# Kernel tuning notes

Measured on AMD Instinct MI355X. Metric: run time of the kernel, lower is better.

Reference implementation:

```python
import jax, jax.numpy as jnp
import numpy as np

D_MODEL = 1024
NUM_HEADS = 16
HEAD_DIM = D_MODEL // NUM_HEADS
SCALE = HEAD_DIM ** -0.5


def setup_inputs() -> dict:
    key = jax.random.key(0)
    k1, k2, k3 = jax.random.split(key, 3)
    x = jax.random.normal(k1, (4, 2048, D_MODEL), dtype=jnp.float32)
    # torch Linear stores weight [out, in]; we store transposed [in, out] for x @ W
    w_qkv = jax.random.normal(k2, (D_MODEL, 3 * D_MODEL), dtype=jnp.float32) * (D_MODEL ** -0.5)
    w_out = jax.random.normal(k3, (D_MODEL, D_MODEL), dtype=jnp.float32) * (D_MODEL ** -0.5)
    return {"x": x, "w_qkv": w_qkv, "w_out": w_out}


def reference(x, w_qkv, w_out):
    batch, seq_len, _ = x.shape
    qkv = x @ w_qkv  # [B, S, 3*D]
    q, k, v = jnp.split(qkv, 3, axis=-1)

    def to_heads(t):
        return t.reshape(batch, seq_len, NUM_HEADS, HEAD_DIM).transpose(0, 2, 1, 3)  # [B, H, S, Dh]

    q, k, v = to_heads(q), to_heads(k), to_heads(v)
    attn = jnp.einsum('bhqd,bhkd->bhqk', q, k) * SCALE  # [B, H, S, S]
    causal = jnp.tril(jnp.ones((seq_len, seq_len), dtype=bool))
    attn = jnp.where(causal[None, None], attn, -jnp.inf)
    attn = jax.nn.softmax(attn, axis=-1)
    out = jnp.einsum('bhqk,bhkd->bhqd', attn, v)  # [B, H, S, Dh]
    out = out.transpose(0, 2, 1, 3).reshape(batch, seq_len, D_MODEL)
    return out @ w_out
```

## Files before the change

### kernel.cpp

```cpp
#include <hip/hip_runtime.h>
#include <hip/hip_bf16.h>

typedef unsigned short u16;
typedef float f32x4 __attribute__((ext_vector_type(4)));
typedef __bf16 bf16x8 __attribute__((ext_vector_type(8)));
typedef u16 u16x8 __attribute__((ext_vector_type(8)));
typedef u16 u16x4 __attribute__((ext_vector_type(4)));
typedef unsigned u32x2 __attribute__((ext_vector_type(2)));

__device__ __forceinline__ u16 f2bf(float f) {
  unsigned u = __builtin_bit_cast(unsigned, f);
  u = (u + 0x7fffu + ((u >> 16) & 1u)) >> 16;
  return (u16)u;
}

__device__ __forceinline__ unsigned cvtpk(float lo, float hi) {
  unsigned r;
  asm("v_cvt_pk_bf16_f32 %0, %1, %2" : "=v"(r) : "v"(lo), "v"(hi));
  return r;
}

__device__ __forceinline__ float exp2b(float x) {
  return __builtin_amdgcn_exp2f(x);
}

__device__ __forceinline__ void gload16(const void* g, void* l) {
  __builtin_amdgcn_global_load_lds(
      (const __attribute__((address_space(1))) unsigned*)g,
      (__attribute__((address_space(3))) unsigned*)l, 16, 0, 0);
}

__device__ __forceinline__ f32x4 mfma16(bf16x8 a, bf16x8 b, f32x4 c) {
  return __builtin_amdgcn_mfma_f32_16x16x32_bf16(a, b, c, 0, 0, 0);
}

__global__ __launch_bounds__(256) void convx(const float4* __restrict__ x,
                                             u16x8* __restrict__ xb, int n) {
  int i = blockIdx.x * 256 + threadIdx.x;
  if (i >= n) return;
  float4 a = x[2 * i], b = x[2 * i + 1];
  u16x8 o;
  o[0] = f2bf(a.x); o[1] = f2bf(a.y); o[2] = f2bf(a.z); o[3] = f2bf(a.w);
  o[4] = f2bf(b.x); o[5] = f2bf(b.y); o[6] = f2bf(b.z); o[7] = f2bf(b.w);
  xb[i] = o;
}

__global__ __launch_bounds__(256) void transpose_w(const float* __restrict__ w,
                                                   u16* __restrict__ wt,
                                                   int R, int C) {
  __shared__ float tile[32][33];
  int n0 = blockIdx.x * 32, k0 = blockIdx.y * 32;
  int tx = threadIdx.x & 31, ty = threadIdx.x >> 5;
#pragma unroll
  for (int j = 0; j < 32; j += 8)
    tile[ty + j][tx] = w[(size_t)(k0 + ty + j) * C + n0 + tx];
  __syncthreads();
#pragma unroll
  for (int j = 0; j < 32; j += 8)
    wt[(size_t)(n0 + ty + j) * R + k0 + tx] = f2bf(tile[tx][ty + j]);
}

template <int MODE, int BM, int BN, int WGM, int WGN, int WPE>
__global__ __launch_bounds__(512, WPE) void gemm_t(const u16* __restrict__ A,
                                                   const u16* __restrict__ Bt,
                                                   void* __restrict__ Cv,
                                                   int M, int N, int K,
                                                   u16* __restrict__ Qb,
                                                   u16* __restrict__ Kb) {
  constexpr int PWM = BM / WGM, PWN = BN / WGN;
  constexpr int MI = PWM / 16;
  constexpr bool PH2 = (MI >= 4);
  constexpr int MH = PH2 ? MI / 2 : MI;
  static_assert(PWN == 64, "per-wave N must be 64 (NI=4)");
  constexpr int ALD = BM / 128, BLD = BN / 128, LPT = ALD + BLD;
  __shared__ alignas(16) u16 As[3][BM][32];
  __shared__ alignas(16) u16 Bs[3][BN][32];
  const int tix = threadIdx.x;
  const int lane = tix & 63, wid = tix >> 6;
  const int wm = wid / WGN, wn = wid % WGN;
  const int r = lane & 15, g = lane >> 4;
  const int s2 = (r >> 1) & 3;
  const int m0 = blockIdx.y * BM, n0 = blockIdx.x * BN;

  const int srow = tix >> 2;
  const int swc = (tix & 3) ^ ((srow >> 1) & 3);
  const u16* gA[ALD];
  const u16* gB[BLD];
#pragma unroll
  for (int i = 0; i < ALD; ++i)
    gA[i] = A + (size_t)(m0 + i * 128 + srow) * K + swc * 8;
#pragma unroll
  for (int i = 0; i < BLD; ++i)
    gB[i] = Bt + (size_t)(n0 + i * 128 + srow) * K + swc * 8;

  auto SA = [&](int tt, int bb) {
    const int ko = tt * 32;
#pragma unroll
    for (int i = 0; i < ALD; ++i)
      gload16(gA[i] + ko, &As[bb][i * 128 + wid * 16][0]);
  };
  auto SB = [&](int tt, int bb) {
    const int ko = tt * 32;
#pragma unroll
    for (int i = 0; i < BLD; ++i)
      gload16(gB[i] + ko, &Bs[bb][i * 128 + wid * 16][0]);
  };

  f32x4 acc[MI][4] = {};
  const int NT = K >> 5;

  SA(0, 0); SB(0, 0); SA(1, 1); SB(1, 1);

  int bu = 0;
  for (int t = 0; t < NT; ++t) {
    if (t < NT - 1) {
      if constexpr (LPT == 3) asm volatile("s_waitcnt vmcnt(3)" ::: "memory");
      else                    asm volatile("s_waitcnt vmcnt(2)" ::: "memory");
    } else {
      asm volatile("s_waitcnt vmcnt(0)" ::: "memory");
    }
    __builtin_amdgcn_s_barrier();
    __builtin_amdgcn_sched_barrier(0);

    const int bs = (bu >= 1) ? bu - 1 : 2;

    bf16x8 a0[MH], bf[4];
#pragma unroll
    for (int mi = 0; mi < MH; ++mi)
      a0[mi] = *(const bf16x8*)&As[bu][wm * PWM + mi * 16 + r][(g ^ s2) * 8];
#pragma unroll
    for (int ni = 0; ni < 4; ++ni)
      bf[ni] = *(const bf16x8*)&Bs[bu][wn * 64 + ni * 16 + r][(g ^ s2) * 8];
    if (t + 2 < NT) SA(t + 2, bs);

    if constexpr (PH2) {
      __builtin_amdgcn_s_barrier();
      asm volatile("s_waitcnt lgkmcnt(0)" ::: "memory");
      __builtin_amdgcn_sched_barrier(0);
      __builtin_amdgcn_s_setprio(1);
#pragma unroll
      for (int mi = 0; mi < MH; ++mi)
#pragma unroll
        for (int ni = 0; ni < 4; ++ni)
          acc[mi][ni] = mfma16(a0[mi], bf[ni], acc[mi][ni]);
      __builtin_amdgcn_s_setprio(0);
      __builtin_amdgcn_s_barrier();

      bf16x8 a1[MH];
#pragma unroll
      for (int mi = 0; mi < MH; ++mi)
        a1[mi] = *(const bf16x8*)&As[bu][wm * PWM + (MH + mi) * 16 + r][(g ^ s2) * 8];
      if (t + 2 < NT) SB(t + 2, bs);
      __builtin_amdgcn_s_barrier();
      asm volatile("s_waitcnt lgkmcnt(0)" ::: "memory");
      __builtin_amdgcn_sched_barrier(0);
      __builtin_amdgcn_s_setprio(1);
#pragma unroll
      for (int mi = 0; mi < MH; ++mi)
#pragma unroll
        for (int ni = 0; ni < 4; ++ni)
          acc[MH + mi][ni] = mfma16(a1[mi], bf[ni], acc[MH + mi][ni]);
      __builtin_amdgcn_s_setprio(0);
    } else {
      if (t + 2 < NT) SB(t + 2, bs);
      __builtin_amdgcn_s_barrier();
      asm volatile("s_waitcnt lgkmcnt(0)" ::: "memory");
      __builtin_amdgcn_sched_barrier(0);
      __builtin_amdgcn_s_setprio(1);
#pragma unroll
      for (int mi = 0; mi < MI; ++mi)
#pragma unroll
        for (int ni = 0; ni < 4; ++ni)
          acc[mi][ni] = mfma16(a0[mi], bf[ni], acc[mi][ni]);
      __builtin_amdgcn_s_setprio(0);
    }
    bu = (bu + 1 >= 3) ? 0 : bu + 1;
  }

#pragma unroll
  for (int mi = 0; mi < MI; ++mi) {
    int row = m0 + wm * PWM + mi * 16 + g * 4;
#pragma unroll
    for (int ni = 0; ni < 4; ++ni) {
      int col = n0 + wn * 64 + ni * 16 + r;
#pragma unroll
      for (int e = 0; e < 4; ++e) {
        float v = acc[mi][ni][e];
        int rr = row + e;
        if (MODE == 0) {
          ((u16*)Cv)[(size_t)rr * N + col] = f2bf(v);
        } else if (MODE == 2) {
          ((float*)Cv)[(size_t)rr * N + col] = v;
        } else {
          int which = col >> 10, hh = (col >> 6) & 15, dd = col & 63;
          int bb = rr >> 11, ss = rr & 2047;
          size_t idx = ((size_t)(bb * 16 + hh) * 2048 + ss) * 64 + dd;
          (which ? Kb : Qb)[idx] = f2bf(which ? v : v * 0.18033688011112042f);
        }
      }
    }
  }
}

__global__ __launch_bounds__(512, 6) void attn_fwd(const u16* __restrict__ Q,
                                                   const u16* __restrict__ Kc,
                                                   const u16* __restrict__ Vt,
                                                   u16* __restrict__ O) {
  __shared__ alignas(16) u16 Ks[2][64][64];
  __shared__ alignas(16) u16 Vs[2][64][64];
  __shared__ alignas(16) u16 Ps[8][16][72];
  const int lane = threadIdx.x & 63, wid = threadIdx.x >> 6;
  const int r = lane & 15, g = lane >> 4;
  const int bh = blockIdx.x, b = bh >> 4, h = bh & 15;
  const int qb = 15 - (int)blockIdx.y;
  const int qw = qb * 128 + wid * 16;
  const int nkv = 2 * (qb + 1);

  const u16* Kp = Kc + (size_t)bh * 2048 * 64;
  const u16* Vp = Vt + (size_t)(h * 64) * 8192 + (size_t)b * 2048;
  const u16* Qp = Q + ((size_t)bh * 2048 + qw) * 64;
  u16* pw = &Ps[wid][0][0];

  const int srow = lane >> 3;
  const int scol = ((lane & 7) ^ srow) * 8;

  bf16x8 qf[2];
  qf[0] = *(const bf16x8*)(Qp + (size_t)r * 64 + g * 8);
  qf[1] = *(const bf16x8*)(Qp + (size_t)r * 64 + 32 + g * 8);

  u16x8 ov8;
#pragma unroll
  for (int i = 0; i < 8; ++i) ov8[i] = 0x3F80;
  const bf16x8 ones = __builtin_bit_cast(bf16x8, ov8);

  f32x4 o[5] = {};

  gload16(Kp + (size_t)(wid * 8 + srow) * 64 + scol, &Ks[0][wid * 8][0]);
  gload16(Vp + (size_t)(wid * 8 + srow) * 8192 + scol, &Vs[0][wid * 8][0]);

  int cur = 0;
  for (int t = 0; t < nkv; ++t, cur ^= 1) {
    __syncthreads();
    if (t + 1 < nkv) {
      const int kn = (t + 1) * 64;
      gload16(Kp + (size_t)(kn + wid * 8 + srow) * 64 + scol, &Ks[cur ^ 1][wid * 8][0]);
      gload16(Vp + (size_t)(wid * 8 + srow) * 8192 + kn + scol, &Vs[cur ^ 1][wid * 8][0]);
    }
    const int kv0 = t * 64;
    if (kv0 > qw + 15) continue;

    f32x4 s[4];
    __builtin_amdgcn_s_setprio(1);
#pragma unroll
    for (int tt = 0; tt < 4; ++tt) {
      bf16x8 k0 = *(const bf16x8*)&Ks[cur][tt * 16 + r][((0 + g) ^ (r & 7)) * 8];
      bf16x8 k1 = *(const bf16x8*)&Ks[cur][tt * 16 + r][((4 + g) ^ (r & 7)) * 8];
      f32x4 z = {-16.f, -16.f, -16.f, -16.f};
      z = mfma16(k0, qf[0], z);
      z = mfma16(k1, qf[1], z);
      s[tt] = z;
    }
    __builtin_amdgcn_s_setprio(0);
    if (kv0 + 63 > qw) {
#pragma unroll
      for (int tt = 0; tt < 4; ++tt) {
        int kvb = kv0 + tt * 16 + g * 4;
#pragma unroll
        for (int e = 0; e < 4; ++e)
          if (kvb + e > qw + r) s[tt][e] = -1e30f;
      }
    }

#pragma unroll
    for (int tt = 0; tt < 4; ++tt) {
      float p0 = exp2b(s[tt][0]), p1 = exp2b(s[tt][1]);
      float p2 = exp2b(s[tt][2]), p3 = exp2b(s[tt][3]);
      u32x2 w;
      w[0] = cvtpk(p0, p1);
      w[1] = cvtpk(p2, p3);
      *(u32x2*)&pw[r * 72 + tt * 16 + g * 4] = w;
    }

    bf16x8 pB0 = *(const bf16x8*)&pw[r * 72 + g * 8];
    bf16x8 pB1 = *(const bf16x8*)&pw[r * 72 + 32 + g * 8];
    __builtin_amdgcn_s_setprio(1);
#pragma unroll
    for (int dt = 0; dt < 4; ++dt) {
      bf16x8 v0 = *(const bf16x8*)&Vs[cur][dt * 16 + r][((0 + g) ^ (r & 7)) * 8];
      bf16x8 v1 = *(const bf16x8*)&Vs[cur][dt * 16 + r][((4 + g) ^ (r & 7)) * 8];
      o[dt] = mfma16(v0, pB0, o[dt]);
      o[dt] = mfma16(v1, pB1, o[dt]);
    }
    o[4] = mfma16(ones, pB0, o[4]);
    o[4] = mfma16(ones, pB1, o[4]);
    __builtin_amdgcn_s_setprio(0);
  }

  float inv = 1.f / o[4][0];
  size_t rowbase = ((size_t)b * 2048 + qw + r) * 1024 + h * 64;
#pragma unroll
  for (int dt = 0; dt < 4; ++dt) {
    u16x4 ov;
#pragma unroll
    for (int e = 0; e < 4; ++e) ov[e] = f2bf(o[dt][e] * inv);
    *(u16x4*)&O[rowbase + dt * 16 + g * 4] = ov;
  }
}

extern "C" void kernel_launch(void* const* d_in, const int* in_sizes, int n_in,
                              void* d_out, int out_size, void* d_ws,
                              size_t ws_size, hipStream_t stream) {
  const float* x = (const float*)d_in[0];
  const float* wqkv = (const float*)d_in[1];
  const float* wout = (const float*)d_in[2];
  float* out = (float*)d_out;
  char* ws = (char*)d_ws;

  u16* Xb = (u16*)ws;
  u16* Wt = (u16*)(ws + (16ull << 20));
  u16* WoT = (u16*)(ws + (22ull << 20));
  u16* Qb = (u16*)(ws + (24ull << 20));
  u16* Kb = (u16*)(ws + (40ull << 20));
  u16* Vt = (u16*)(ws + (56ull << 20));

  convx<<<4096, 256, 0, stream>>>((const float4*)x, (u16x8*)Xb, 1048576);
  transpose_w<<<dim3(96, 32), 256, 0, stream>>>(wqkv, Wt, 1024, 3072);
  transpose_w<<<dim3(32, 32), 256, 0, stream>>>(wout, WoT, 1024, 1024);

  gemm_t<1, 256, 128, 4, 2, 4><<<dim3(16, 32), 512, 0, stream>>>(
      Xb, Wt, nullptr, 8192, 2048, 1024, Qb, Kb);
  gemm_t<0, 128, 128, 4, 2, 6><<<dim3(64, 8), 512, 0, stream>>>(
      Wt + (size_t)2048 * 1024, Xb, Vt, 1024, 8192, 1024, nullptr, nullptr);
  attn_fwd<<<dim3(64, 16), 512, 0, stream>>>(Qb, Kb, Vt, Xb);
  gemm_t<2, 128, 128, 4, 2, 6><<<dim3(8, 64), 512, 0, stream>>>(
      Xb, WoT, out, 8192, 1024, 1024, nullptr, nullptr);
}
```

Before: 155.3 us.

## Replace LDS double buffer with register prefetch and single K/V buffer

The attention kernel stops using a double-buffered LDS layout filled by direct global-to-LDS loads. It now prefetches the next K/V tile into registers during compute and writes it to a single LDS buffer after a barrier. This halves K/V shared-memory usage, and the launch-bounds occupancy hint rises from 6 to 8 blocks. The cost is two barriers per iteration instead of one, plus extra VGPRs for the staged tile.

```diff
diff --git a/kernel.cpp b/kernel.cpp
--- a/kernel.cpp
+++ b/kernel.cpp
@@ -7,6 +7,7 @@
 typedef u16 u16x8 __attribute__((ext_vector_type(8)));
 typedef u16 u16x4 __attribute__((ext_vector_type(4)));
 typedef unsigned u32x2 __attribute__((ext_vector_type(2)));
+typedef unsigned u32x4 __attribute__((ext_vector_type(4)));
 
 __device__ __forceinline__ u16 f2bf(float f) {
   unsigned u = __builtin_bit_cast(unsigned, f);
@@ -202,12 +203,12 @@
   }
 }
 
-__global__ __launch_bounds__(512, 6) void attn_fwd(const u16* __restrict__ Q,
+__global__ __launch_bounds__(512, 8) void attn_fwd(const u16* __restrict__ Q,
                                                    const u16* __restrict__ Kc,
                                                    const u16* __restrict__ Vt,
                                                    u16* __restrict__ O) {
-  __shared__ alignas(16) u16 Ks[2][64][64];
-  __shared__ alignas(16) u16 Vs[2][64][64];
+  __shared__ alignas(16) u16 Ks[64][64];
+  __shared__ alignas(16) u16 Vs[64][64];
   __shared__ alignas(16) u16 Ps[8][16][72];
   const int lane = threadIdx.x & 63, wid = threadIdx.x >> 6;
   const int r = lane & 15, g = lane >> 4;
@@ -223,6 +224,11 @@
 
   const int srow = lane >> 3;
   const int scol = ((lane & 7) ^ srow) * 8;
+  const int myrow = wid * 8 + srow;
+  u16* kdst = &Ks[myrow][(lane & 7) * 8];
+  u16* vdst = &Vs[myrow][(lane & 7) * 8];
+  const u16* kgp = Kp + (size_t)myrow * 64 + scol;
+  const u16* vgp = Vp + (size_t)myrow * 8192 + scol;
 
   bf16x8 qf[2];
   qf[0] = *(const bf16x8*)(Qp + (size_t)r * 64 + g * 8);
@@ -235,65 +241,74 @@
 
   f32x4 o[5] = {};
 
-  gload16(Kp + (size_t)(wid * 8 + srow) * 64 + scol, &Ks[0][wid * 8][0]);
-  gload16(Vp + (size_t)(wid * 8 + srow) * 8192 + scol, &Vs[0][wid * 8][0]);
-
-  int cur = 0;
-  for (int t = 0; t < nkv; ++t, cur ^= 1) {
+  {
+    u32x4 k0 = *(const u32x4*)kgp;
+    u32x4 v0 = *(const u32x4*)vgp;
+    *(u32x4*)kdst = k0;
+    *(u32x4*)vdst = v0;
+  }
+  __syncthreads();
+
+  u32x4 kreg, vreg;
+  for (int t = 0; t < nkv; ++t) {
+    if (t + 1 < nkv) {
+      kreg = *(const u32x4*)(kgp + (size_t)(t + 1) * 64 * 64);
+      vreg = *(const u32x4*)(vgp + (t + 1) * 64);
+    }
+    const int kv0 = t * 64;
+    if (kv0 <= qw + 15) {
+      f32x4 s[4];
+      __builtin_amdgcn_s_setprio(1);
+#pragma unroll
+      for (int tt = 0; tt < 4; ++tt) {
+        bf16x8 k0 = *(const bf16x8*)&Ks[tt * 16 + r][((0 + g) ^ (r & 7)) * 8];
+        bf16x8 k1 = *(const bf16x8*)&Ks[tt * 16 + r][((4 + g) ^ (r & 7)) * 8];
+        f32x4 z = {-16.f, -16.f, -16.f, -16.f};
+        z = mfma16(k0, qf[0], z);
+        z = mfma16(k1, qf[1], z);
+        s[tt] = z;
+      }
+      __builtin_amdgcn_s_setprio(0);
+      if (kv0 + 63 > qw) {
+#pragma unroll
+        for (int tt = 0; tt < 4; ++tt) {
+          int kvb = kv0 + tt * 16 + g * 4;
+#pragma unroll
+          for (int e = 0; e < 4; ++e)
+            if (kvb + e > qw + r) s[tt][e] = -1e30f;
+        }
+      }
+
+#pragma unroll
+      for (int tt = 0; tt < 4; ++tt) {
+        float p0 = exp2b(s[tt][0]), p1 = exp2b(s[tt][1]);
+        float p2 = exp2b(s[tt][2]), p3 = exp2b(s[tt][3]);
+        u32x2 w;
+        w[0] = cvtpk(p0, p1);
+        w[1] = cvtpk(p2, p3);
+        *(u32x2*)&pw[r * 72 + tt * 16 + g * 4] = w;
+      }
+
+      bf16x8 pB0 = *(const bf16x8*)&pw[r * 72 + g * 8];
+      bf16x8 pB1 = *(const bf16x8*)&pw[r * 72 + 32 + g * 8];
+      __builtin_amdgcn_s_setprio(1);
+#pragma unroll
+      for (int dt = 0; dt < 4; ++dt) {
+        bf16x8 v0 = *(const bf16x8*)&Vs[dt * 16 + r][((0 + g) ^ (r & 7)) * 8];
+        bf16x8 v1 = *(const bf16x8*)&Vs[dt * 16 + r][((4 + g) ^ (r & 7)) * 8];
+        o[dt] = mfma16(v0, pB0, o[dt]);
+        o[dt] = mfma16(v1, pB1, o[dt]);
+      }
+      o[4] = mfma16(ones, pB0, o[4]);
+      o[4] = mfma16(ones, pB1, o[4]);
+      __builtin_amdgcn_s_setprio(0);
+    }
     __syncthreads();
     if (t + 1 < nkv) {
-      const int kn = (t + 1) * 64;
-      gload16(Kp + (size_t)(kn + wid * 8 + srow) * 64 + scol, &Ks[cur ^ 1][wid * 8][0]);
-      gload16(Vp + (size_t)(wid * 8 + srow) * 8192 + kn + scol, &Vs[cur ^ 1][wid * 8][0]);
-    }
-    const int kv0 = t * 64;
-    if (kv0 > qw + 15) continue;
-
-    f32x4 s[4];
-    __builtin_amdgcn_s_setprio(1);
-#pragma unroll
-    for (int tt = 0; tt < 4; ++tt) {
-      bf16x8 k0 = *(const bf16x8*)&Ks[cur][tt * 16 + r][((0 + g) ^ (r & 7)) * 8];
-      bf16x8 k1 = *(const bf16x8*)&Ks[cur][tt * 16 + r][((4 + g) ^ (r & 7)) * 8];
-      f32x4 z = {-16.f, -16.f, -16.f, -16.f};
-      z = mfma16(k0, qf[0], z);
-      z = mfma16(k1, qf[1], z);
-      s[tt] = z;
-    }
-    __builtin_amdgcn_s_setprio(0);
-    if (kv0 + 63 > qw) {
-#pragma unroll
-      for (int tt = 0; tt < 4; ++tt) {
-        int kvb = kv0 + tt * 16 + g * 4;
-#pragma unroll
-        for (int e = 0; e < 4; ++e)
-          if (kvb + e > qw + r) s[tt][e] = -1e30f;
-      }
-    }
-
-#pragma unroll
-    for (int tt = 0; tt < 4; ++tt) {
-      float p0 = exp2b(s[tt][0]), p1 = exp2b(s[tt][1]);
-      float p2 = exp2b(s[tt][2]), p3 = exp2b(s[tt][3]);
-      u32x2 w;
-      w[0] = cvtpk(p0, p1);
-      w[1] = cvtpk(p2, p3);
-      *(u32x2*)&pw[r * 72 + tt * 16 + g * 4] = w;
-    }
-
-    bf16x8 pB0 = *(const bf16x8*)&pw[r * 72 + g * 8];
-    bf16x8 pB1 = *(const bf16x8*)&pw[r * 72 + 32 + g * 8];
-    __builtin_amdgcn_s_setprio(1);
-#pragma unroll
-    for (int dt = 0; dt < 4; ++dt) {
-      bf16x8 v0 = *(const bf16x8*)&Vs[cur][dt * 16 + r][((0 + g) ^ (r & 7)) * 8];
-      bf16x8 v1 = *(const bf16x8*)&Vs[cur][dt * 16 + r][((4 + g) ^ (r & 7)) * 8];
-      o[dt] = mfma16(v0, pB0, o[dt]);
-      o[dt] = mfma16(v1, pB1, o[dt]);
-    }
-    o[4] = mfma16(ones, pB0, o[4]);
-    o[4] = mfma16(ones, pB1, o[4]);
-    __builtin_amdgcn_s_setprio(0);
+      *(u32x4*)kdst = kreg;
+      *(u32x4*)vdst = vreg;
+    }
+    __syncthreads();
   }
 
   float inv = 1.f / o[4][0];
```

Result: slower. 202.5 us (+30.4%).
